# Performance work log

Hardware: AMD Instinct MI355X
Metric: run time of the kernel (lower is better)

The kernel has to match this reference:

```python
import jax, jax.numpy as jnp
import numpy as np

N_NODES = 100000
N_EDGES = 800000
IN_SIZE = 128
OUT_SIZE = 64
DEPTH = 2


def setup_inputs() -> dict:
    key = jax.random.key(0)
    k1, k2, k3, k4, k5 = jax.random.split(key, 5)
    data = jax.random.normal(k1, (N_NODES, IN_SIZE), dtype=jnp.float32)
    W = jax.random.normal(k2, (IN_SIZE, OUT_SIZE), dtype=jnp.float32) * (1.0 / np.sqrt(IN_SIZE))
    b = jax.random.normal(k3, (OUT_SIZE,), dtype=jnp.float32) * 0.01
    src_idx = jax.random.randint(k4, (N_EDGES,), 0, N_NODES, dtype=jnp.int64)
    tgt_idx = jnp.sort(jax.random.randint(k5, (N_EDGES,), 0, N_NODES, dtype=jnp.int64))
    return {"data": data, "W": W, "b": b, "src_idx": src_idx, "tgt_idx": tgt_idx}


def reference(data, W, b, src_idx, tgt_idx):
    # GCN(X,S) = relu( A_S^depth (X W + b) )
    out = data @ W + b  # [N, out_size]
    n = data.shape[0]
    # per-target edge counts (message_size); same every depth iteration
    counts = jax.ops.segment_sum(jnp.ones_like(tgt_idx, dtype=out.dtype), tgt_idx, num_segments=n)
    m = counts[tgt_idx][:, None]  # [E, 1], >= 1 wherever indexed
    for _ in range(DEPTH):
        # own/(m*(m+1)) summed over m edges of a node == own/(m+1);
        # plus sum of sources/(m+1): mean-style normalization
        msg = out[tgt_idx] / (m * (m + 1.0)) + out[src_idx] / (m + 1.0)
        out = jax.ops.segment_sum(msg, tgt_idx, num_segments=n)
    return jax.nn.relu(out)
```

## Files before the change

kernel.cpp:

```cpp
#include <hip/hip_runtime.h>

#define N_NODES 100000
#define N_EDGES 800000
#define IN_SIZE 128
#define OUT_SIZE 64

#define RP_BLOCKS   ((N_EDGES + 255) / 256)
#define GEMM_BLOCKS 1024
#define N_TILES     (N_NODES / 16)
#define PROP_BLOCKS ((N_NODES + 63) / 64)
#define WS 136

typedef __attribute__((ext_vector_type(8))) short short8;
typedef __attribute__((ext_vector_type(4))) float f32x4;

__device__ __forceinline__ unsigned short f2bf(float x) {
    unsigned u = __float_as_uint(x);
    u += 0x7FFFu + ((u >> 16) & 1u);
    return (unsigned short)(u >> 16);
}
__device__ __forceinline__ unsigned pack2(float lo, float hi) {
    return (unsigned)f2bf(lo) | ((unsigned)f2bf(hi) << 16);
}


__global__ __launch_bounds__(256) void gemm_rowptr_kernel(
    const float* __restrict__ data, const float* __restrict__ W,
    const float* __restrict__ b, const int* __restrict__ tgt,
    uint4* __restrict__ H, float* __restrict__ Hs, int* __restrict__ rowptr)
{
    if (blockIdx.x < RP_BLOCKS) {
        const int e = (int)blockIdx.x * 256 + (int)threadIdx.x;
        if (e < N_EDGES) {
            const int bb = tgt[e];
            const int a  = (e == 0) ? -1 : tgt[e - 1];
            for (int t = a + 1; t <= bb; ++t) rowptr[t] = e;
            if (e == N_EDGES - 1)
                for (int t = bb + 1; t <= N_NODES; ++t) rowptr[t] = N_EDGES;
        }
        return;
    }

    __shared__ __align__(16) unsigned short Wt[64 * WS];
    __shared__ unsigned Clds[4][16 * 20];

    const int tid  = threadIdx.x;
    const int lane = tid & 63;
    const int wv   = tid >> 6;
    const int quad = lane >> 4;
    const int col  = lane & 15;

    {
        const int p = tid & 63;
        const int h = tid >> 6;
        const float* w0 = W + (size_t)(2 * p) * OUT_SIZE + h * 16;
        const float* w1 = w0 + OUT_SIZE;
        unsigned* Wt32 = (unsigned*)Wt;
        #pragma unroll
        for (int i = 0; i < 16; ++i)
            Wt32[(h * 16 + i) * (WS / 2) + p] = pack2(w0[i], w1[i]);
    }
    __syncthreads();

    float bcol[4];
    #pragma unroll
    for (int nt = 0; nt < 4; ++nt) bcol[nt] = b[nt * 16 + col];

    short8 wb[4][4];
    #pragma unroll
    for (int kc = 0; kc < 4; ++kc)
        #pragma unroll
        for (int nt = 0; nt < 4; ++nt)
            wb[kc][nt] = *(const short8*)(
                Wt + (nt * 16 + col) * WS + kc * 32 + quad * 8);

    union U8 { short8 v; unsigned short u[8]; };
    unsigned* cl = Clds[wv];

    for (int tile = ((int)blockIdx.x - RP_BLOCKS) * 4 + wv; tile < N_TILES;
         tile += GEMM_BLOCKS * 4) {
        const int r0 = tile * 16;
        const float* arow = data + (size_t)(r0 + col) * IN_SIZE + quad * 8;

        short8 af[4];
        #pragma unroll
        for (int kc = 0; kc < 4; ++kc) {
            const float4 x0 = *(const float4*)(arow + kc * 32);
            const float4 x1 = *(const float4*)(arow + kc * 32 + 4);
            U8 t;
            t.u[0] = f2bf(x0.x); t.u[1] = f2bf(x0.y);
            t.u[2] = f2bf(x0.z); t.u[3] = f2bf(x0.w);
            t.u[4] = f2bf(x1.x); t.u[5] = f2bf(x1.y);
            t.u[6] = f2bf(x1.z); t.u[7] = f2bf(x1.w);
            af[kc] = t.v;
        }

        f32x4 acc[4];
        #pragma unroll
        for (int nt = 0; nt < 4; ++nt) acc[nt] = (f32x4){0.f, 0.f, 0.f, 0.f};
        #pragma unroll
        for (int kc = 0; kc < 4; ++kc) {
            #pragma unroll
            for (int nt = 0; nt < 4; ++nt)
                acc[nt] = __builtin_amdgcn_mfma_f32_16x16x32_bf16(
                    af[kc], wb[kc][nt], acc[nt], 0, 0, 0);
        }

        float v[4][4];
        #pragma unroll
        for (int nt = 0; nt < 4; ++nt)
            #pragma unroll
            for (int r = 0; r < 4; ++r)
                v[nt][r] = acc[nt][r] + bcol[nt];

        float rmax[4];
        #pragma unroll
        for (int r = 0; r < 4; ++r) {
            float m = fabsf(v[0][r]);
            m = fmaxf(m, fabsf(v[1][r]));
            m = fmaxf(m, fabsf(v[2][r]));
            m = fmaxf(m, fabsf(v[3][r]));
            m = fmaxf(m, __shfl_xor(m, 1, 64));
            m = fmaxf(m, __shfl_xor(m, 2, 64));
            m = fmaxf(m, __shfl_xor(m, 4, 64));
            m = fmaxf(m, __shfl_xor(m, 8, 64));
            rmax[r] = m;
        }
        if (col < 4)
            Hs[r0 + quad * 4 + col] = rmax[col] * (1.f / 127.f);

        #pragma unroll
        for (int r = 0; r < 4; ++r) {
            const float inv = rmax[r] > 0.f ? 127.f / rmax[r] : 0.f;
            const unsigned u0 = (unsigned)(int)rintf(v[0][r] * inv + 128.f);
            const unsigned u1 = (unsigned)(int)rintf(v[1][r] * inv + 128.f);
            const unsigned u2 = (unsigned)(int)rintf(v[2][r] * inv + 128.f);
            const unsigned u3 = (unsigned)(int)rintf(v[3][r] * inv + 128.f);
            cl[(quad * 4 + r) * 20 + col] =
                u0 | (u1 << 8) | (u2 << 16) | (u3 << 24);
        }

        {
            const int row = lane >> 2;
            const int seg = lane & 3;
            const uint4 vv = *(const uint4*)(cl + row * 20 + seg * 4);
            H[(size_t)(r0 + row) * 4 + seg] = vv;
        }
    }
}

#define ACC16(vv, c)                                                        \
    {                                                                        \
        const unsigned* _w = (const unsigned*)&(vv);                         \
        _Pragma("unroll")                                                    \
        for (int _d = 0; _d < 4; ++_d) {                                     \
            _Pragma("unroll")                                                \
            for (int _b = 0; _b < 4; ++_b)                                   \
                acc[_d * 4 + _b] = fmaf(                                     \
                    (float)((_w[_d] >> (8 * _b)) & 255u), (c), acc[_d*4+_b]);\
        }                                                                    \
    }

template <bool FINAL>
__global__ __launch_bounds__(256, 6) void prop_kernel(
    const uint4* __restrict__ inq, const float* __restrict__ insc,
    void* __restrict__ outp, float* __restrict__ outsc,
    const int* __restrict__ rowptr, const int* __restrict__ src)
{
    const int tid   = threadIdx.x;
    const int lane  = tid & 63;
    const int s     = lane & 3;
    const int lbase = lane & 60;
    const int noder = blockIdx.x * 64 + (tid >> 2);
    const bool valid = noder < N_NODES;
    const int node  = valid ? noder : N_NODES - 1;

    const int start = rowptr[node];
    const int end   = rowptr[node + 1];
    const int deg   = end - start;

    float acc[16];
    #pragma unroll
    for (int k = 0; k < 16; ++k) acc[k] = 0.f;
    float sumS = 0.f;

    if (deg > 0) {
        {
            const uint4 ownq = inq[(size_t)node * 4 + s];
            const float owns = insc[node];
            ACC16(ownq, owns);
            sumS = owns;
        }
        for (int base = start; base < end; base += 8) {
            const int rem = end - base;
            const int liA = base + s;
            const int svA = src[liA < end ? liA : base];
            int svB = 0;
            if (base + 4 < end) {
                const int liB = base + 4 + s;
                svB = src[liB < end ? liB : base + 4];
            }
            const int e0 = __shfl(svA, lbase + 0, 64);
            const int e1 = __shfl(svA, lbase + 1, 64);
            const int e2 = __shfl(svA, lbase + 2, 64);
            const int e3 = __shfl(svA, lbase + 3, 64);
            const int e4 = __shfl(svB, lbase + 0, 64);
            const int e5 = __shfl(svB, lbase + 1, 64);
            const int e6 = __shfl(svB, lbase + 2, 64);
            const int e7 = __shfl(svB, lbase + 3, 64);

            const int i1 = rem > 1 ? e1 : e0;
            const int i2 = rem > 2 ? e2 : e0;
            const int i3 = rem > 3 ? e3 : e0;
            const int i4 = rem > 4 ? e4 : e0;
            const int i5 = rem > 5 ? e5 : e0;
            const int i6 = rem > 6 ? e6 : e0;
            const int i7 = rem > 7 ? e7 : e0;

            const uint4 v0 = inq[(size_t)e0 * 4 + s];
            const uint4 v1 = inq[(size_t)i1 * 4 + s];
            const uint4 v2 = inq[(size_t)i2 * 4 + s];
            const uint4 v3 = inq[(size_t)i3 * 4 + s];
            const uint4 v4 = inq[(size_t)i4 * 4 + s];
            const uint4 v5 = inq[(size_t)i5 * 4 + s];
            const uint4 v6 = inq[(size_t)i6 * 4 + s];
            const uint4 v7 = inq[(size_t)i7 * 4 + s];

            const float c0 = insc[e0];
            const float c1 = rem > 1 ? insc[i1] : 0.f;
            const float c2 = rem > 2 ? insc[i2] : 0.f;
            const float c3 = rem > 3 ? insc[i3] : 0.f;
            const float c4 = rem > 4 ? insc[i4] : 0.f;
            const float c5 = rem > 5 ? insc[i5] : 0.f;
            const float c6 = rem > 6 ? insc[i6] : 0.f;
            const float c7 = rem > 7 ? insc[i7] : 0.f;

            sumS += (c0 + c1) + (c2 + c3) + ((c4 + c5) + (c6 + c7));
            ACC16(v0, c0); ACC16(v1, c1); ACC16(v2, c2); ACC16(v3, c3);
            ACC16(v4, c4); ACC16(v5, c5); ACC16(v6, c6); ACC16(v7, c7);
        }
    }

    float val[16];
    if (deg == 0) {
        #pragma unroll
        for (int k = 0; k < 16; ++k) val[k] = 0.f;
    } else {
        const float invm  = 1.0f / (float)(deg + 1);
        const float bias  = 128.f * sumS;
        #pragma unroll
        for (int k = 0; k < 16; ++k) {
            val[k] = (acc[k] - bias) * invm;
            if (FINAL) val[k] = fmaxf(val[k], 0.f);
        }
    }

    if (FINAL) {
        __shared__ float T[64 * 68];
        const int nl = tid >> 2;
        #pragma unroll
        for (int d = 0; d < 4; ++d)
            #pragma unroll
            for (int bb = 0; bb < 4; ++bb)
                T[nl * 68 + (s * 4 + d) + 16 * bb] = val[d * 4 + bb];
        __syncthreads();
        float* out = (float*)outp;
        const int nb = blockIdx.x * 64;
        #pragma unroll
        for (int p = 0; p < 4; ++p) {
            const int pos = p * 1024 + tid * 4;
            const int n   = pos >> 6;
            const int ch  = pos & 63;
            if (nb + n < N_NODES) {
                const float4 vv = *(const float4*)(T + n * 68 + ch);
                *(float4*)(out + (size_t)(nb + n) * OUT_SIZE + ch) = vv;
            }
        }
    } else {
        float m = 0.f;
        #pragma unroll
        for (int k = 0; k < 16; ++k) m = fmaxf(m, fabsf(val[k]));
        m = fmaxf(m, __shfl_xor(m, 1, 64));
        m = fmaxf(m, __shfl_xor(m, 2, 64));
        const float invq = m > 0.f ? 127.f / m : 0.f;
        uint4 pv;
        unsigned* pw = (unsigned*)&pv;
        #pragma unroll
        for (int d = 0; d < 4; ++d) {
            const unsigned u0 = (unsigned)(int)rintf(val[d * 4 + 0] * invq + 128.f);
            const unsigned u1 = (unsigned)(int)rintf(val[d * 4 + 1] * invq + 128.f);
            const unsigned u2 = (unsigned)(int)rintf(val[d * 4 + 2] * invq + 128.f);
            const unsigned u3 = (unsigned)(int)rintf(val[d * 4 + 3] * invq + 128.f);
            pw[d] = u0 | (u1 << 8) | (u2 << 16) | (u3 << 24);
        }
        if (valid) {
            ((uint4*)outp)[(size_t)node * 4 + s] = pv;
            if (s == 0) outsc[node] = m * (1.f / 127.f);
        }
    }
}

extern "C" void kernel_launch(void* const* d_in, const int* in_sizes, int n_in,
                              void* d_out, int out_size, void* d_ws, size_t ws_size,
                              hipStream_t stream)
{
    const float* data = (const float*)d_in[0];
    const float* W    = (const float*)d_in[1];
    const float* b    = (const float*)d_in[2];
    const int*   src  = (const int*)d_in[3];
    const int*   tgt  = (const int*)d_in[4];

    char*  base   = (char*)d_ws;
    uint4* H0     = (uint4*)base;
    uint4* H1     = (uint4*)(base + (size_t)N_NODES * OUT_SIZE);
    float* H0s    = (float*)(base + 2 * (size_t)N_NODES * OUT_SIZE);
    float* H1s    = H0s + N_NODES;
    int*   rowptr = (int*)(H1s + N_NODES);

    gemm_rowptr_kernel<<<RP_BLOCKS + GEMM_BLOCKS, 256, 0, stream>>>(
        data, W, b, tgt, H0, H0s, rowptr);
    prop_kernel<false><<<PROP_BLOCKS, 256, 0, stream>>>(
        H0, H0s, (void*)H1, H1s, rowptr, src);
    prop_kernel<true ><<<PROP_BLOCKS, 256, 0, stream>>>(
        H1, H1s, d_out, nullptr, rowptr, src);
}
```

Baseline: 146.7 us.

## Fuse GEMM, rowptr and two propagation passes into one cooperative persistent kernel

```diff
diff --git a/kernel.cpp b/kernel.cpp
--- a/kernel.cpp
+++ b/kernel.cpp
@@ -1,14 +1,16 @@
 #include <hip/hip_runtime.h>
+#include <hip/hip_cooperative_groups.h>
+
+namespace cg = cooperative_groups;
 
 #define N_NODES 100000
 #define N_EDGES 800000
 #define IN_SIZE 128
 #define OUT_SIZE 64
 
-#define RP_BLOCKS   ((N_EDGES + 255) / 256)
-#define GEMM_BLOCKS 1024
+#define RP_CHUNKS   ((N_EDGES + 255) / 256)
 #define N_TILES     (N_NODES / 16)
-#define PROP_BLOCKS ((N_NODES + 63) / 64)
+#define PROP_CHUNKS ((N_NODES + 63) / 64)
 #define WS 136
 
 typedef __attribute__((ext_vector_type(8))) short short8;
@@ -23,131 +25,6 @@
     return (unsigned)f2bf(lo) | ((unsigned)f2bf(hi) << 16);
 }
 
-
-__global__ __launch_bounds__(256) void gemm_rowptr_kernel(
-    const float* __restrict__ data, const float* __restrict__ W,
-    const float* __restrict__ b, const int* __restrict__ tgt,
-    uint4* __restrict__ H, float* __restrict__ Hs, int* __restrict__ rowptr)
-{
-    if (blockIdx.x < RP_BLOCKS) {
-        const int e = (int)blockIdx.x * 256 + (int)threadIdx.x;
-        if (e < N_EDGES) {
-            const int bb = tgt[e];
-            const int a  = (e == 0) ? -1 : tgt[e - 1];
-            for (int t = a + 1; t <= bb; ++t) rowptr[t] = e;
-            if (e == N_EDGES - 1)
-                for (int t = bb + 1; t <= N_NODES; ++t) rowptr[t] = N_EDGES;
-        }
-        return;
-    }
-
-    __shared__ __align__(16) unsigned short Wt[64 * WS];
-    __shared__ unsigned Clds[4][16 * 20];
-
-    const int tid  = threadIdx.x;
-    const int lane = tid & 63;
-    const int wv   = tid >> 6;
-    const int quad = lane >> 4;
-    const int col  = lane & 15;
-
-    {
-        const int p = tid & 63;
-        const int h = tid >> 6;
-        const float* w0 = W + (size_t)(2 * p) * OUT_SIZE + h * 16;
-        const float* w1 = w0 + OUT_SIZE;
-        unsigned* Wt32 = (unsigned*)Wt;
-        #pragma unroll
-        for (int i = 0; i < 16; ++i)
-            Wt32[(h * 16 + i) * (WS / 2) + p] = pack2(w0[i], w1[i]);
-    }
-    __syncthreads();
-
-    float bcol[4];
-    #pragma unroll
-    for (int nt = 0; nt < 4; ++nt) bcol[nt] = b[nt * 16 + col];
-
-    short8 wb[4][4];
-    #pragma unroll
-    for (int kc = 0; kc < 4; ++kc)
-        #pragma unroll
-        for (int nt = 0; nt < 4; ++nt)
-            wb[kc][nt] = *(const short8*)(
-                Wt + (nt * 16 + col) * WS + kc * 32 + quad * 8);
-
-    union U8 { short8 v; unsigned short u[8]; };
-    unsigned* cl = Clds[wv];
-
-    for (int tile = ((int)blockIdx.x - RP_BLOCKS) * 4 + wv; tile < N_TILES;
-         tile += GEMM_BLOCKS * 4) {
-        const int r0 = tile * 16;
-        const float* arow = data + (size_t)(r0 + col) * IN_SIZE + quad * 8;
-
-        short8 af[4];
-        #pragma unroll
-        for (int kc = 0; kc < 4; ++kc) {
-            const float4 x0 = *(const float4*)(arow + kc * 32);
-            const float4 x1 = *(const float4*)(arow + kc * 32 + 4);
-            U8 t;
-            t.u[0] = f2bf(x0.x); t.u[1] = f2bf(x0.y);
-            t.u[2] = f2bf(x0.z); t.u[3] = f2bf(x0.w);
-            t.u[4] = f2bf(x1.x); t.u[5] = f2bf(x1.y);
-            t.u[6] = f2bf(x1.z); t.u[7] = f2bf(x1.w);
-            af[kc] = t.v;
-        }
-
-        f32x4 acc[4];
-        #pragma unroll
-        for (int nt = 0; nt < 4; ++nt) acc[nt] = (f32x4){0.f, 0.f, 0.f, 0.f};
-        #pragma unroll
-        for (int kc = 0; kc < 4; ++kc) {
-            #pragma unroll
-            for (int nt = 0; nt < 4; ++nt)
-                acc[nt] = __builtin_amdgcn_mfma_f32_16x16x32_bf16(
-                    af[kc], wb[kc][nt], acc[nt], 0, 0, 0);
-        }
-
-        float v[4][4];
-        #pragma unroll
-        for (int nt = 0; nt < 4; ++nt)
-            #pragma unroll
-            for (int r = 0; r < 4; ++r)
-                v[nt][r] = acc[nt][r] + bcol[nt];
-
-        float rmax[4];
-        #pragma unroll
-        for (int r = 0; r < 4; ++r) {
-            float m = fabsf(v[0][r]);
-            m = fmaxf(m, fabsf(v[1][r]));
-            m = fmaxf(m, fabsf(v[2][r]));
-            m = fmaxf(m, fabsf(v[3][r]));
-            m = fmaxf(m, __shfl_xor(m, 1, 64));
-            m = fmaxf(m, __shfl_xor(m, 2, 64));
-            m = fmaxf(m, __shfl_xor(m, 4, 64));
-            m = fmaxf(m, __shfl_xor(m, 8, 64));
-            rmax[r] = m;
-        }
-        if (col < 4)
-            Hs[r0 + quad * 4 + col] = rmax[col] * (1.f / 127.f);
-
-        #pragma unroll
-        for (int r = 0; r < 4; ++r) {
-            const float inv = rmax[r] > 0.f ? 127.f / rmax[r] : 0.f;
-            const unsigned u0 = (unsigned)(int)rintf(v[0][r] * inv + 128.f);
-            const unsigned u1 = (unsigned)(int)rintf(v[1][r] * inv + 128.f);
-            const unsigned u2 = (unsigned)(int)rintf(v[2][r] * inv + 128.f);
-            const unsigned u3 = (unsigned)(int)rintf(v[3][r] * inv + 128.f);
-            cl[(quad * 4 + r) * 20 + col] =
-                u0 | (u1 << 8) | (u2 << 16) | (u3 << 24);
-        }
-
-        {
-            const int row = lane >> 2;
-            const int seg = lane & 3;
-            const uint4 vv = *(const uint4*)(cl + row * 20 + seg * 4);
-            H[(size_t)(r0 + row) * 4 + seg] = vv;
-        }
-    }
-}
 
 #define ACC16(vv, c)                                                        \
     {                                                                        \
@@ -161,143 +38,283 @@
         }                                                                    \
     }
 
+struct __align__(16) SMem {
+    union {
+        struct { unsigned short Wt[64 * WS]; unsigned Clds[4][16 * 20]; } g;
+        float T[64 * 68];
+    };
+};
+
 template <bool FINAL>
-__global__ __launch_bounds__(256, 6) void prop_kernel(
+__device__ __forceinline__ void prop_phase(
     const uint4* __restrict__ inq, const float* __restrict__ insc,
-    void* __restrict__ outp, float* __restrict__ outsc,
-    const int* __restrict__ rowptr, const int* __restrict__ src)
+    uint4* __restrict__ outq, float* __restrict__ outsc,
+    float* __restrict__ out, const int* __restrict__ rowptr,
+    const int* __restrict__ src, float* __restrict__ T, int G)
 {
     const int tid   = threadIdx.x;
     const int lane  = tid & 63;
     const int s     = lane & 3;
     const int lbase = lane & 60;
-    const int noder = blockIdx.x * 64 + (tid >> 2);
-    const bool valid = noder < N_NODES;
-    const int node  = valid ? noder : N_NODES - 1;
-
-    const int start = rowptr[node];
-    const int end   = rowptr[node + 1];
-    const int deg   = end - start;
-
-    float acc[16];
-    #pragma unroll
-    for (int k = 0; k < 16; ++k) acc[k] = 0.f;
-    float sumS = 0.f;
-
-    if (deg > 0) {
-        {
-            const uint4 ownq = inq[(size_t)node * 4 + s];
-            const float owns = insc[node];
-            ACC16(ownq, owns);
-            sumS = owns;
-        }
-        for (int base = start; base < end; base += 8) {
-            const int rem = end - base;
-            const int liA = base + s;
-            const int svA = src[liA < end ? liA : base];
-            int svB = 0;
-            if (base + 4 < end) {
-                const int liB = base + 4 + s;
-                svB = src[liB < end ? liB : base + 4];
-            }
-            const int e0 = __shfl(svA, lbase + 0, 64);
-            const int e1 = __shfl(svA, lbase + 1, 64);
-            const int e2 = __shfl(svA, lbase + 2, 64);
-            const int e3 = __shfl(svA, lbase + 3, 64);
-            const int e4 = __shfl(svB, lbase + 0, 64);
-            const int e5 = __shfl(svB, lbase + 1, 64);
-            const int e6 = __shfl(svB, lbase + 2, 64);
-            const int e7 = __shfl(svB, lbase + 3, 64);
-
-            const int i1 = rem > 1 ? e1 : e0;
-            const int i2 = rem > 2 ? e2 : e0;
-            const int i3 = rem > 3 ? e3 : e0;
-            const int i4 = rem > 4 ? e4 : e0;
-            const int i5 = rem > 5 ? e5 : e0;
-            const int i6 = rem > 6 ? e6 : e0;
-            const int i7 = rem > 7 ? e7 : e0;
-
-            const uint4 v0 = inq[(size_t)e0 * 4 + s];
-            const uint4 v1 = inq[(size_t)i1 * 4 + s];
-            const uint4 v2 = inq[(size_t)i2 * 4 + s];
-            const uint4 v3 = inq[(size_t)i3 * 4 + s];
-            const uint4 v4 = inq[(size_t)i4 * 4 + s];
-            const uint4 v5 = inq[(size_t)i5 * 4 + s];
-            const uint4 v6 = inq[(size_t)i6 * 4 + s];
-            const uint4 v7 = inq[(size_t)i7 * 4 + s];
-
-            const float c0 = insc[e0];
-            const float c1 = rem > 1 ? insc[i1] : 0.f;
-            const float c2 = rem > 2 ? insc[i2] : 0.f;
-            const float c3 = rem > 3 ? insc[i3] : 0.f;
-            const float c4 = rem > 4 ? insc[i4] : 0.f;
-            const float c5 = rem > 5 ? insc[i5] : 0.f;
-            const float c6 = rem > 6 ? insc[i6] : 0.f;
-            const float c7 = rem > 7 ? insc[i7] : 0.f;
-
-            sumS += (c0 + c1) + (c2 + c3) + ((c4 + c5) + (c6 + c7));
-            ACC16(v0, c0); ACC16(v1, c1); ACC16(v2, c2); ACC16(v3, c3);
-            ACC16(v4, c4); ACC16(v5, c5); ACC16(v6, c6); ACC16(v7, c7);
-        }
-    }
-
-    float val[16];
-    if (deg == 0) {
+
+    for (int nb = (int)blockIdx.x; nb < PROP_CHUNKS; nb += G) {
+        const int noder = nb * 64 + (tid >> 2);
+        const bool valid = noder < N_NODES;
+        const int node  = valid ? noder : N_NODES - 1;
+
+        const int start = rowptr[node];
+        const int end   = rowptr[node + 1];
+        const int deg   = end - start;
+
+        float acc[16];
         #pragma unroll
-        for (int k = 0; k < 16; ++k) val[k] = 0.f;
-    } else {
-        const float invm  = 1.0f / (float)(deg + 1);
-        const float bias  = 128.f * sumS;
+        for (int k = 0; k < 16; ++k) acc[k] = 0.f;
+        float sumS = 0.f;
+
+        if (deg > 0) {
+            {
+                const uint4 ownq = inq[(size_t)node * 4 + s];
+                const float owns = insc[node];
+                ACC16(ownq, owns);
+                sumS = owns;
+            }
+            for (int base = start; base < end; base += 8) {
+                const int rem = end - base;
+                const int liA = base + s;
+                const int svA = src[liA < end ? liA : base];
+                int svB = 0;
+                if (base + 4 < end) {
+                    const int liB = base + 4 + s;
+                    svB = src[liB < end ? liB : base + 4];
+                }
+                const int e0 = __shfl(svA, lbase + 0, 64);
+                const int e1 = __shfl(svA, lbase + 1, 64);
+                const int e2 = __shfl(svA, lbase + 2, 64);
+                const int e3 = __shfl(svA, lbase + 3, 64);
+                const int e4 = __shfl(svB, lbase + 0, 64);
+                const int e5 = __shfl(svB, lbase + 1, 64);
+                const int e6 = __shfl(svB, lbase + 2, 64);
+                const int e7 = __shfl(svB, lbase + 3, 64);
+
+                const int i1 = rem > 1 ? e1 : e0;
+                const int i2 = rem > 2 ? e2 : e0;
+                const int i3 = rem > 3 ? e3 : e0;
+                const int i4 = rem > 4 ? e4 : e0;
+                const int i5 = rem > 5 ? e5 : e0;
+                const int i6 = rem > 6 ? e6 : e0;
+                const int i7 = rem > 7 ? e7 : e0;
+
+                const uint4 v0 = inq[(size_t)e0 * 4 + s];
+                const uint4 v1 = inq[(size_t)i1 * 4 + s];
+                const uint4 v2 = inq[(size_t)i2 * 4 + s];
+                const uint4 v3 = inq[(size_t)i3 * 4 + s];
+                const uint4 v4 = inq[(size_t)i4 * 4 + s];
+                const uint4 v5 = inq[(size_t)i5 * 4 + s];
+                const uint4 v6 = inq[(size_t)i6 * 4 + s];
+                const uint4 v7 = inq[(size_t)i7 * 4 + s];
+
+                const float c0 = insc[e0];
+                const float c1 = rem > 1 ? insc[i1] : 0.f;
+                const float c2 = rem > 2 ? insc[i2] : 0.f;
+                const float c3 = rem > 3 ? insc[i3] : 0.f;
+                const float c4 = rem > 4 ? insc[i4] : 0.f;
+                const float c5 = rem > 5 ? insc[i5] : 0.f;
+                const float c6 = rem > 6 ? insc[i6] : 0.f;
+                const float c7 = rem > 7 ? insc[i7] : 0.f;
+
+                sumS += (c0 + c1) + (c2 + c3) + ((c4 + c5) + (c6 + c7));
+                ACC16(v0, c0); ACC16(v1, c1); ACC16(v2, c2); ACC16(v3, c3);
+                ACC16(v4, c4); ACC16(v5, c5); ACC16(v6, c6); ACC16(v7, c7);
+            }
+        }
+
+        float val[16];
+        if (deg == 0) {
+            #pragma unroll
+            for (int k = 0; k < 16; ++k) val[k] = 0.f;
+        } else {
+            const float invm  = 1.0f / (float)(deg + 1);
+            const float bias  = 128.f * sumS;
+            #pragma unroll
+            for (int k = 0; k < 16; ++k) {
+                val[k] = (acc[k] - bias) * invm;
+                if (FINAL) val[k] = fmaxf(val[k], 0.f);
+            }
+        }
+
+        if (FINAL) {
+            const int nl = tid >> 2;
+            #pragma unroll
+            for (int d = 0; d < 4; ++d)
+                #pragma unroll
+                for (int bb = 0; bb < 4; ++bb)
+                    T[nl * 68 + (s * 4 + d) + 16 * bb] = val[d * 4 + bb];
+            __syncthreads();
+            const int nbase = nb * 64;
+            #pragma unroll
+            for (int p = 0; p < 4; ++p) {
+                const int pos = p * 1024 + tid * 4;
+                const int n   = pos >> 6;
+                const int ch  = pos & 63;
+                if (nbase + n < N_NODES) {
+                    const float4 vv = *(const float4*)(T + n * 68 + ch);
+                    *(float4*)(out + (size_t)(nbase + n) * OUT_SIZE + ch) = vv;
+                }
+            }
+            __syncthreads();
+        } else {
+            float m = 0.f;
+            #pragma unroll
+            for (int k = 0; k < 16; ++k) m = fmaxf(m, fabsf(val[k]));
+            m = fmaxf(m, __shfl_xor(m, 1, 64));
+            m = fmaxf(m, __shfl_xor(m, 2, 64));
+            const float invq = m > 0.f ? 127.f / m : 0.f;
+            uint4 pv;
+            unsigned* pw = (unsigned*)&pv;
+            #pragma unroll
+            for (int d = 0; d < 4; ++d) {
+                const unsigned u0 = (unsigned)(int)rintf(val[d * 4 + 0] * invq + 128.f);
+                const unsigned u1 = (unsigned)(int)rintf(val[d * 4 + 1] * invq + 128.f);
+                const unsigned u2 = (unsigned)(int)rintf(val[d * 4 + 2] * invq + 128.f);
+                const unsigned u3 = (unsigned)(int)rintf(val[d * 4 + 3] * invq + 128.f);
+                pw[d] = u0 | (u1 << 8) | (u2 << 16) | (u3 << 24);
+            }
+            if (valid) {
+                outq[(size_t)node * 4 + s] = pv;
+                if (s == 0) outsc[node] = m * (1.f / 127.f);
+            }
+        }
+    }
+}
+
+__global__ __launch_bounds__(256, 4) void gcn_fused(
+    const float* __restrict__ data, const float* __restrict__ W,
+    const float* __restrict__ b, const int* __restrict__ src,
+    const int* __restrict__ tgt,
+    uint4* __restrict__ H0, float* __restrict__ H0s,
+    uint4* __restrict__ H1, float* __restrict__ H1s,
+    int* __restrict__ rowptr, float* __restrict__ out)
+{
+    cg::grid_group grid = cg::this_grid();
+    const int G   = (int)gridDim.x;
+    const int tid = (int)threadIdx.x;
+
+    __shared__ SMem sm;
+
+    for (int c = (int)blockIdx.x; c < RP_CHUNKS; c += G) {
+        const int e = c * 256 + tid;
+        if (e < N_EDGES) {
+            const int bb = tgt[e];
+            const int a  = (e == 0) ? -1 : tgt[e - 1];
+            for (int t = a + 1; t <= bb; ++t) rowptr[t] = e;
+            if (e == N_EDGES - 1)
+                for (int t = bb + 1; t <= N_NODES; ++t) rowptr[t] = N_EDGES;
+        }
+    }
+
+    {
+        const int p = tid & 63;
+        const int h = tid >> 6;
+        const float* w0 = W + (size_t)(2 * p) * OUT_SIZE + h * 16;
+        const float* w1 = w0 + OUT_SIZE;
+        unsigned* Wt32 = (unsigned*)sm.g.Wt;
         #pragma unroll
-        for (int k = 0; k < 16; ++k) {
-            val[k] = (acc[k] - bias) * invm;
-            if (FINAL) val[k] = fmaxf(val[k], 0.f);
-        }
-    }
-
-    if (FINAL) {
-        __shared__ float T[64 * 68];
-        const int nl = tid >> 2;
+        for (int i = 0; i < 16; ++i)
+            Wt32[(h * 16 + i) * (WS / 2) + p] = pack2(w0[i], w1[i]);
+    }
+    __syncthreads();
+
+    {
+        const int lane = tid & 63;
+        const int wv   = tid >> 6;
+        const int quad = lane >> 4;
+        const int col  = lane & 15;
+
+        float bcol[4];
         #pragma unroll
-        for (int d = 0; d < 4; ++d)
-            #pragma unroll
-            for (int bb = 0; bb < 4; ++bb)
-                T[nl * 68 + (s * 4 + d) + 16 * bb] = val[d * 4 + bb];
-        __syncthreads();
-        float* out = (float*)outp;
-        const int nb = blockIdx.x * 64;
-        #pragma unroll
-        for (int p = 0; p < 4; ++p) {
-            const int pos = p * 1024 + tid * 4;
-            const int n   = pos >> 6;
-            const int ch  = pos & 63;
-            if (nb + n < N_NODES) {
-                const float4 vv = *(const float4*)(T + n * 68 + ch);
-                *(float4*)(out + (size_t)(nb + n) * OUT_SIZE + ch) = vv;
-            }
-        }
-    } else {
-        float m = 0.f;
-        #pragma unroll
-        for (int k = 0; k < 16; ++k) m = fmaxf(m, fabsf(val[k]));
-        m = fmaxf(m, __shfl_xor(m, 1, 64));
-        m = fmaxf(m, __shfl_xor(m, 2, 64));
-        const float invq = m > 0.f ? 127.f / m : 0.f;
-        uint4 pv;
-        unsigned* pw = (unsigned*)&pv;
-        #pragma unroll
-        for (int d = 0; d < 4; ++d) {
-            const unsigned u0 = (unsigned)(int)rintf(val[d * 4 + 0] * invq + 128.f);
-            const unsigned u1 = (unsigned)(int)rintf(val[d * 4 + 1] * invq + 128.f);
-            const unsigned u2 = (unsigned)(int)rintf(val[d * 4 + 2] * invq + 128.f);
-            const unsigned u3 = (unsigned)(int)rintf(val[d * 4 + 3] * invq + 128.f);
-            pw[d] = u0 | (u1 << 8) | (u2 << 16) | (u3 << 24);
-        }
-        if (valid) {
-            ((uint4*)outp)[(size_t)node * 4 + s] = pv;
-            if (s == 0) outsc[node] = m * (1.f / 127.f);
-        }
-    }
+        for (int nt = 0; nt < 4; ++nt) bcol[nt] = b[nt * 16 + col];
+
+        union U8 { short8 v; unsigned short u[8]; };
+        unsigned* cl = sm.g.Clds[wv];
+
+        for (int tile = (int)blockIdx.x * 4 + wv; tile < N_TILES; tile += G * 4) {
+            const int r0 = tile * 16;
+            const float* arow = data + (size_t)(r0 + col) * IN_SIZE + quad * 8;
+
+            f32x4 acc[4];
+            #pragma unroll
+            for (int nt = 0; nt < 4; ++nt) acc[nt] = (f32x4){0.f, 0.f, 0.f, 0.f};
+
+            #pragma unroll
+            for (int kc = 0; kc < 4; ++kc) {
+                const float4 x0 = *(const float4*)(arow + kc * 32);
+                const float4 x1 = *(const float4*)(arow + kc * 32 + 4);
+                U8 t;
+                t.u[0] = f2bf(x0.x); t.u[1] = f2bf(x0.y);
+                t.u[2] = f2bf(x0.z); t.u[3] = f2bf(x0.w);
+                t.u[4] = f2bf(x1.x); t.u[5] = f2bf(x1.y);
+                t.u[6] = f2bf(x1.z); t.u[7] = f2bf(x1.w);
+                #pragma unroll
+                for (int nt = 0; nt < 4; ++nt) {
+                    const short8 wb = *(const short8*)(
+                        sm.g.Wt + (nt * 16 + col) * WS + kc * 32 + quad * 8);
+                    acc[nt] = __builtin_amdgcn_mfma_f32_16x16x32_bf16(
+                        t.v, wb, acc[nt], 0, 0, 0);
+                }
+            }
+
+            float v[4][4];
+            #pragma unroll
+            for (int nt = 0; nt < 4; ++nt)
+                #pragma unroll
+                for (int r = 0; r < 4; ++r)
+                    v[nt][r] = acc[nt][r] + bcol[nt];
+
+            float rmax[4];
+            #pragma unroll
+            for (int r = 0; r < 4; ++r) {
+                float m = fabsf(v[0][r]);
+                m = fmaxf(m, fabsf(v[1][r]));
+                m = fmaxf(m, fabsf(v[2][r]));
+                m = fmaxf(m, fabsf(v[3][r]));
+                m = fmaxf(m, __shfl_xor(m, 1, 64));
+                m = fmaxf(m, __shfl_xor(m, 2, 64));
+                m = fmaxf(m, __shfl_xor(m, 4, 64));
+                m = fmaxf(m, __shfl_xor(m, 8, 64));
+                rmax[r] = m;
+            }
+            if (col < 4)
+                H0s[r0 + quad * 4 + col] = rmax[col] * (1.f / 127.f);
+
+            #pragma unroll
+            for (int r = 0; r < 4; ++r) {
+                const float inv = rmax[r] > 0.f ? 127.f / rmax[r] : 0.f;
+                const unsigned u0 = (unsigned)(int)rintf(v[0][r] * inv + 128.f);
+                const unsigned u1 = (unsigned)(int)rintf(v[1][r] * inv + 128.f);
+                const unsigned u2 = (unsigned)(int)rintf(v[2][r] * inv + 128.f);
+                const unsigned u3 = (unsigned)(int)rintf(v[3][r] * inv + 128.f);
+                cl[(quad * 4 + r) * 20 + col] =
+                    u0 | (u1 << 8) | (u2 << 16) | (u3 << 24);
+            }
+
+            {
+                const int row = lane >> 2;
+                const int seg = lane & 3;
+                const uint4 vv = *(const uint4*)(cl + row * 20 + seg * 4);
+                H0[(size_t)(r0 + row) * 4 + seg] = vv;
+            }
+        }
+    }
+
+    __threadfence();
+    grid.sync();
+
+    prop_phase<false>(H0, H0s, H1, H1s, nullptr, rowptr, src, sm.T, G);
+
+    __threadfence();
+    grid.sync();
+
+    prop_phase<true>(H1, H1s, nullptr, nullptr, out, rowptr, src, sm.T, G);
 }
 
 extern "C" void kernel_launch(void* const* d_in, const int* in_sizes, int n_in,
@@ -316,11 +333,23 @@
     float* H0s    = (float*)(base + 2 * (size_t)N_NODES * OUT_SIZE);
     float* H1s    = H0s + N_NODES;
     int*   rowptr = (int*)(H1s + N_NODES);
-
-    gemm_rowptr_kernel<<<RP_BLOCKS + GEMM_BLOCKS, 256, 0, stream>>>(
-        data, W, b, tgt, H0, H0s, rowptr);
-    prop_kernel<false><<<PROP_BLOCKS, 256, 0, stream>>>(
-        H0, H0s, (void*)H1, H1s, rowptr, src);
-    prop_kernel<true ><<<PROP_BLOCKS, 256, 0, stream>>>(
-        H1, H1s, d_out, nullptr, rowptr, src);
-}
+    float* out    = (float*)d_out;
+
+    static int g_blocks = 0;
+    if (g_blocks == 0) {
+        int maxb = 0;
+        if (hipOccupancyMaxActiveBlocksPerMultiprocessor(
+                &maxb, gcn_fused, 256, 0) != hipSuccess || maxb <= 0)
+            maxb = 2;
+        g_blocks = maxb * 256;
+        if (g_blocks > 2048) g_blocks = 2048;
+    }
+
+    void* args[] = {
+        (void*)&data, (void*)&W, (void*)&b, (void*)&src, (void*)&tgt,
+        (void*)&H0, (void*)&H0s, (void*)&H1, (void*)&H1s,
+        (void*)&rowptr, (void*)&out
+    };
+    hipLaunchCooperativeKernel((const void*)gcn_fused, dim3(g_blocks),
+                               dim3(256), args, 0, stream);
+}
```

After: 360.6 us. +145.8%, slower.

## Split quantized feature table into two channel halves for smaller gather footprint

Applied to the files above, without the earlier changes.

```diff
diff --git a/kernel.cpp b/kernel.cpp
--- a/kernel.cpp
+++ b/kernel.cpp
@@ -13,6 +13,8 @@
 
 typedef __attribute__((ext_vector_type(8))) short short8;
 typedef __attribute__((ext_vector_type(4))) float f32x4;
+typedef __attribute__((ext_vector_type(4))) unsigned u32x4;
+typedef __attribute__((ext_vector_type(2))) unsigned u32x2;
 
 __device__ __forceinline__ unsigned short f2bf(float x) {
     unsigned u = __float_as_uint(x);
@@ -27,7 +29,8 @@
 __global__ __launch_bounds__(256) void gemm_rowptr_kernel(
     const float* __restrict__ data, const float* __restrict__ W,
     const float* __restrict__ b, const int* __restrict__ tgt,
-    uint4* __restrict__ H, float* __restrict__ Hs, int* __restrict__ rowptr)
+    unsigned* __restrict__ H0a, unsigned* __restrict__ H0b,
+    float* __restrict__ Hs, int* __restrict__ rowptr)
 {
     if (blockIdx.x < RP_BLOCKS) {
         const int e = (int)blockIdx.x * 256 + (int)threadIdx.x;
@@ -143,28 +146,32 @@
         {
             const int row = lane >> 2;
             const int seg = lane & 3;
-            const uint4 vv = *(const uint4*)(cl + row * 20 + seg * 4);
-            H[(size_t)(r0 + row) * 4 + seg] = vv;
-        }
-    }
-}
-
-#define ACC16(vv, c)                                                        \
+            const u32x4 vv = *(const u32x4*)(cl + row * 20 + seg * 4);
+            unsigned* pl = (seg & 2) ? H0b : H0a;
+            __builtin_nontemporal_store(vv,
+                (u32x4*)(pl + (size_t)(r0 + row) * 8 + (seg & 1) * 4));
+        }
+    }
+}
+
+#define ACC8(vv, c)                                                         \
     {                                                                        \
-        const unsigned* _w = (const unsigned*)&(vv);                         \
+        const unsigned _wx = (vv).x, _wy = (vv).y;                           \
         _Pragma("unroll")                                                    \
-        for (int _d = 0; _d < 4; ++_d) {                                     \
-            _Pragma("unroll")                                                \
-            for (int _b = 0; _b < 4; ++_b)                                   \
-                acc[_d * 4 + _b] = fmaf(                                     \
-                    (float)((_w[_d] >> (8 * _b)) & 255u), (c), acc[_d*4+_b]);\
+        for (int _b = 0; _b < 4; ++_b) {                                     \
+            acc[_b]     = fmaf((float)((_wx >> (8 * _b)) & 255u), (c),       \
+                               acc[_b]);                                     \
+            acc[4 + _b] = fmaf((float)((_wy >> (8 * _b)) & 255u), (c),       \
+                               acc[4 + _b]);                                 \
         }                                                                    \
     }
 
 template <bool FINAL>
-__global__ __launch_bounds__(256, 6) void prop_kernel(
-    const uint4* __restrict__ inq, const float* __restrict__ insc,
-    void* __restrict__ outp, float* __restrict__ outsc,
+__global__ __launch_bounds__(256) void prop_half_kernel(
+    const uint2* __restrict__ inq,
+    const float* __restrict__ insc,
+    unsigned* __restrict__ outq, float* __restrict__ outsc,
+    float* __restrict__ out, int choff,
     const int* __restrict__ rowptr, const int* __restrict__ src)
 {
     const int tid   = threadIdx.x;
@@ -179,26 +186,28 @@
     const int end   = rowptr[node + 1];
     const int deg   = end - start;
 
-    float acc[16];
+    float acc[8];
     #pragma unroll
-    for (int k = 0; k < 16; ++k) acc[k] = 0.f;
+    for (int k = 0; k < 8; ++k) acc[k] = 0.f;
     float sumS = 0.f;
 
     if (deg > 0) {
         {
-            const uint4 ownq = inq[(size_t)node * 4 + s];
+            const uint2 ownq = inq[(size_t)node * 4 + s];
             const float owns = insc[node];
-            ACC16(ownq, owns);
+            ACC8(ownq, owns);
             sumS = owns;
         }
         for (int base = start; base < end; base += 8) {
             const int rem = end - base;
             const int liA = base + s;
-            const int svA = src[liA < end ? liA : base];
+            const int svA = __builtin_nontemporal_load(
+                &src[liA < end ? liA : base]);
             int svB = 0;
             if (base + 4 < end) {
                 const int liB = base + 4 + s;
-                svB = src[liB < end ? liB : base + 4];
+                svB = __builtin_nontemporal_load(
+                    &src[liB < end ? liB : base + 4]);
             }
             const int e0 = __shfl(svA, lbase + 0, 64);
             const int e1 = __shfl(svA, lbase + 1, 64);
@@ -217,14 +226,14 @@
             const int i6 = rem > 6 ? e6 : e0;
             const int i7 = rem > 7 ? e7 : e0;
 
-            const uint4 v0 = inq[(size_t)e0 * 4 + s];
-            const uint4 v1 = inq[(size_t)i1 * 4 + s];
-            const uint4 v2 = inq[(size_t)i2 * 4 + s];
-            const uint4 v3 = inq[(size_t)i3 * 4 + s];
-            const uint4 v4 = inq[(size_t)i4 * 4 + s];
-            const uint4 v5 = inq[(size_t)i5 * 4 + s];
-            const uint4 v6 = inq[(size_t)i6 * 4 + s];
-            const uint4 v7 = inq[(size_t)i7 * 4 + s];
+            const uint2 v0 = inq[(size_t)e0 * 4 + s];
+            const uint2 v1 = inq[(size_t)i1 * 4 + s];
+            const uint2 v2 = inq[(size_t)i2 * 4 + s];
+            const uint2 v3 = inq[(size_t)i3 * 4 + s];
+            const uint2 v4 = inq[(size_t)i4 * 4 + s];
+            const uint2 v5 = inq[(size_t)i5 * 4 + s];
+            const uint2 v6 = inq[(size_t)i6 * 4 + s];
+            const uint2 v7 = inq[(size_t)i7 * 4 + s];
 
             const float c0 = insc[e0];
             const float c1 = rem > 1 ? insc[i1] : 0.f;
@@ -236,65 +245,70 @@
             const float c7 = rem > 7 ? insc[i7] : 0.f;
 
             sumS += (c0 + c1) + (c2 + c3) + ((c4 + c5) + (c6 + c7));
-            ACC16(v0, c0); ACC16(v1, c1); ACC16(v2, c2); ACC16(v3, c3);
-            ACC16(v4, c4); ACC16(v5, c5); ACC16(v6, c6); ACC16(v7, c7);
-        }
-    }
-
-    float val[16];
+            ACC8(v0, c0); ACC8(v1, c1); ACC8(v2, c2); ACC8(v3, c3);
+            ACC8(v4, c4); ACC8(v5, c5); ACC8(v6, c6); ACC8(v7, c7);
+        }
+    }
+
+    float val[8];
     if (deg == 0) {
         #pragma unroll
-        for (int k = 0; k < 16; ++k) val[k] = 0.f;
+        for (int k = 0; k < 8; ++k) val[k] = 0.f;
     } else {
         const float invm  = 1.0f / (float)(deg + 1);
         const float bias  = 128.f * sumS;
         #pragma unroll
-        for (int k = 0; k < 16; ++k) {
+        for (int k = 0; k < 8; ++k) {
             val[k] = (acc[k] - bias) * invm;
             if (FINAL) val[k] = fmaxf(val[k], 0.f);
         }
     }
 
     if (FINAL) {
-        __shared__ float T[64 * 68];
+        __shared__ __align__(16) float T[64 * 36];
         const int nl = tid >> 2;
         #pragma unroll
-        for (int d = 0; d < 4; ++d)
+        for (int j = 0; j < 2; ++j)
             #pragma unroll
             for (int bb = 0; bb < 4; ++bb)
-                T[nl * 68 + (s * 4 + d) + 16 * bb] = val[d * 4 + bb];
+                T[nl * 36 + (2 * s + j) + 8 * bb] = val[j * 4 + bb];
         __syncthreads();
-        float* out = (float*)outp;
         const int nb = blockIdx.x * 64;
         #pragma unroll
-        for (int p = 0; p < 4; ++p) {
-            const int pos = p * 1024 + tid * 4;
-            const int n   = pos >> 6;
-            const int ch  = pos & 63;
+        for (int p = 0; p < 2; ++p) {
+            const int f4 = p * 256 + tid;
+            const int n  = f4 >> 3;
+            const int q  = f4 & 7;
             if (nb + n < N_NODES) {
-                const float4 vv = *(const float4*)(T + n * 68 + ch);
-                *(float4*)(out + (size_t)(nb + n) * OUT_SIZE + ch) = vv;
+                const f32x4 vv = *(const f32x4*)(T + n * 36 + q * 4);
+                const int ch = 4 * (q & 1) + choff + 16 * (q >> 1);
+                __builtin_nontemporal_store(vv,
+                    (f32x4*)(out + (size_t)(nb + n) * OUT_SIZE + ch));
             }
         }
     } else {
         float m = 0.f;
         #pragma unroll
-        for (int k = 0; k < 16; ++k) m = fmaxf(m, fabsf(val[k]));
+        for (int k = 0; k < 8; ++k) m = fmaxf(m, fabsf(val[k]));
         m = fmaxf(m, __shfl_xor(m, 1, 64));
         m = fmaxf(m, __shfl_xor(m, 2, 64));
         const float invq = m > 0.f ? 127.f / m : 0.f;
-        uint4 pv;
-        unsigned* pw = (unsigned*)&pv;
-        #pragma unroll
-        for (int d = 0; d < 4; ++d) {
-            const unsigned u0 = (unsigned)(int)rintf(val[d * 4 + 0] * invq + 128.f);
-            const unsigned u1 = (unsigned)(int)rintf(val[d * 4 + 1] * invq + 128.f);
-            const unsigned u2 = (unsigned)(int)rintf(val[d * 4 + 2] * invq + 128.f);
-            const unsigned u3 = (unsigned)(int)rintf(val[d * 4 + 3] * invq + 128.f);
-            pw[d] = u0 | (u1 << 8) | (u2 << 16) | (u3 << 24);
+        u32x2 pv;
+        {
+            const unsigned a0 = (unsigned)(int)rintf(val[0] * invq + 128.f);
+            const unsigned a1 = (unsigned)(int)rintf(val[1] * invq + 128.f);
+            const unsigned a2 = (unsigned)(int)rintf(val[2] * invq + 128.f);
+            const unsigned a3 = (unsigned)(int)rintf(val[3] * invq + 128.f);
+            pv.x = a0 | (a1 << 8) | (a2 << 16) | (a3 << 24);
+            const unsigned b0 = (unsigned)(int)rintf(val[4] * invq + 128.f);
+            const unsigned b1 = (unsigned)(int)rintf(val[5] * invq + 128.f);
+            const unsigned b2 = (unsigned)(int)rintf(val[6] * invq + 128.f);
+            const unsigned b3 = (unsigned)(int)rintf(val[7] * invq + 128.f);
+            pv.y = b0 | (b1 << 8) | (b2 << 16) | (b3 << 24);
         }
         if (valid) {
-            ((uint4*)outp)[(size_t)node * 4 + s] = pv;
+            __builtin_nontemporal_store(pv,
+                (u32x2*)(outq + (size_t)node * 8 + s * 2));
             if (s == 0) outsc[node] = m * (1.f / 127.f);
         }
     }
@@ -310,17 +324,26 @@
     const int*   src  = (const int*)d_in[3];
     const int*   tgt  = (const int*)d_in[4];
 
-    char*  base   = (char*)d_ws;
-    uint4* H0     = (uint4*)base;
-    uint4* H1     = (uint4*)(base + (size_t)N_NODES * OUT_SIZE);
-    float* H0s    = (float*)(base + 2 * (size_t)N_NODES * OUT_SIZE);
-    float* H1s    = H0s + N_NODES;
-    int*   rowptr = (int*)(H1s + N_NODES);
+    unsigned* H0a = (unsigned*)d_ws;
+    unsigned* H0b = H0a + (size_t)N_NODES * 8;
+    unsigned* H1a = H0b + (size_t)N_NODES * 8;
+    unsigned* H1b = H1a + (size_t)N_NODES * 8;
+    float* H0s    = (float*)(H1b + (size_t)N_NODES * 8);
+    float* H1s0   = H0s + N_NODES;
+    float* H1s1   = H1s0 + N_NODES;
+    int*   rowptr = (int*)(H1s1 + N_NODES);
+    float* out    = (float*)d_out;
 
     gemm_rowptr_kernel<<<RP_BLOCKS + GEMM_BLOCKS, 256, 0, stream>>>(
-        data, W, b, tgt, H0, H0s, rowptr);
-    prop_kernel<false><<<PROP_BLOCKS, 256, 0, stream>>>(
-        H0, H0s, (void*)H1, H1s, rowptr, src);
-    prop_kernel<true ><<<PROP_BLOCKS, 256, 0, stream>>>(
-        H1, H1s, d_out, nullptr, rowptr, src);
-}
+        data, W, b, tgt, H0a, H0b, H0s, rowptr);
+
+    prop_half_kernel<false><<<PROP_BLOCKS, 256, 0, stream>>>(
+        (const uint2*)H0a, H0s, H1a, H1s0, nullptr, 0, rowptr, src);
+    prop_half_kernel<false><<<PROP_BLOCKS, 256, 0, stream>>>(
+        (const uint2*)H0b, H0s, H1b, H1s1, nullptr, 8, rowptr, src);
+
+    prop_half_kernel<true><<<PROP_BLOCKS, 256, 0, stream>>>(
+        (const uint2*)H1a, H1s0, nullptr, nullptr, out, 0, rowptr, src);
+    prop_half_kernel<true><<<PROP_BLOCKS, 256, 0, stream>>>(
+        (const uint2*)H1b, H1s1, nullptr, nullptr, out, 8, rowptr, src);
+}
```

New measurement: 177.7 us. 21.1% more time.
